# Kernel tuning notes

Measured on AMD Instinct MI355X. Metric: run time of the kernel, lower is better.

## Reference

```python
import jax, jax.numpy as jnp
import numpy as np
import math

D_MODEL = 1024
N_HEAD = 16
FFN_HIDDEN = 4096
EPS = 1e-12


def _layernorm(x, gamma, beta):
    # faithful to repo: unbiased std (ddof=1), divide by (std + eps)
    mean = jnp.mean(x, axis=-1, keepdims=True)
    std = jnp.std(x, axis=-1, keepdims=True, ddof=1)
    return gamma * ((x - mean) / (std + EPS)) + beta


def setup_inputs() -> dict:
    key = jax.random.key(0)
    ks = jax.random.split(key, 12)
    B, L, D, H = 2, 2048, D_MODEL, FFN_HIDDEN
    s = 0.02
    inp = {
        "x": jax.random.normal(ks[0], (B, L, D), dtype=jnp.float32),
        "src_mask": jnp.ones((B, 1, 1, L), dtype=jnp.int32),
        "wq_w": jax.random.normal(ks[1], (D, D), jnp.float32) * s,
        "wq_b": jnp.zeros((D,), jnp.float32),
        "wk_w": jax.random.normal(ks[2], (D, D), jnp.float32) * s,
        "wk_b": jnp.zeros((D,), jnp.float32),
        "wv_w": jax.random.normal(ks[3], (D, D), jnp.float32) * s,
        "wv_b": jnp.zeros((D,), jnp.float32),
        "wo_w": jax.random.normal(ks[4], (D, D), jnp.float32) * s,
        "wo_b": jnp.zeros((D,), jnp.float32),
        "gamma1": jnp.ones((D,), jnp.float32),
        "beta1": jnp.zeros((D,), jnp.float32),
        "ff1_w": jax.random.normal(ks[5], (D, H), jnp.float32) * s,
        "ff1_b": jnp.zeros((H,), jnp.float32),
        "ff2_w": jax.random.normal(ks[6], (H, D), jnp.float32) * s,
        "ff2_b": jnp.zeros((D,), jnp.float32),
        "gamma2": jnp.ones((D,), jnp.float32),
        "beta2": jnp.zeros((D,), jnp.float32),
    }
    return inp


def _encoder_layer(x, src_mask, wq_w, wq_b, wk_w, wk_b, wv_w, wv_b, wo_w, wo_b,
                   gamma1, beta1, ff1_w, ff1_b, ff2_w, ff2_b, gamma2, beta2):
    B, L, D = x.shape
    H = N_HEAD
    d_t = D // H
    # projections
    q = x @ wq_w + wq_b
    k = x @ wk_w + wk_b
    v = x @ wv_w + wv_b
    # faithful .view() split: reshape [B,L,D] -> [B,H,L,d_t] (no transpose)
    q = q.reshape(B, H, L, d_t)
    k = k.reshape(B, H, L, d_t)
    v = v.reshape(B, H, L, d_t)
    score = jnp.einsum("bhqd,bhkd->bhqk", q, k) / math.sqrt(d_t)
    score = jnp.where(src_mask == 0, jnp.float32(-1e-12), score)
    score = jax.nn.softmax(score, axis=-1)
    out = jnp.einsum("bhqk,bhkd->bhqd", score, v)
    out = out.reshape(B, L, D)  # faithful .view() concat
    attn = out @ wo_w + wo_b
    # residual + LN1 (dropout p=0)
    x1 = _layernorm(attn + x, gamma1, beta1)
    # FFN
    ff = jax.nn.relu(x1 @ ff1_w + ff1_b) @ ff2_w + ff2_b
    return _layernorm(ff + x1, gamma2, beta2)


def reference(x, src_mask, wq_w, wq_b, wk_w, wk_b, wv_w, wv_b, wo_w, wo_b,
              gamma1, beta1, ff1_w, ff1_b, ff2_w, ff2_b, gamma2, beta2):
    return _encoder_layer(x, src_mask, wq_w, wq_b, wk_w, wk_b, wv_w, wv_b,
                          wo_w, wo_b, gamma1, beta1, ff1_w, ff1_b, ff2_w,
                          ff2_b, gamma2, beta2)
```

## Files before the change

### kernel.cpp

```cpp
#include <hip/hip_runtime.h>
#include <hip/hip_bf16.h>
#include <cstdint>
#include <cstddef>

using bf16 = __hip_bfloat16;
typedef __attribute__((ext_vector_type(8))) short short8v;
typedef __attribute__((ext_vector_type(4))) short short4v;
typedef __attribute__((ext_vector_type(4))) float float4v;

__device__ inline float b2f(short s) {
  union { float f; uint32_t u; } z; z.u = ((uint32_t)(uint16_t)s) << 16; return z.f;
}
__device__ inline short f2b(float f) {
  bf16 h = __float2bfloat16(f);
  return *reinterpret_cast<short*>(&h);
}

typedef const __attribute__((address_space(1))) uint32_t* gas1p;
typedef __attribute__((address_space(3))) uint32_t* las3p;
__device__ inline void gload_lds16(const void* g, void* l) {
  __builtin_amdgcn_global_load_lds((gas1p)g, (las3p)l, 16, 0, 0);
}

__global__ __launch_bounds__(256) void gemm_bt(
    const bf16* __restrict__ A, const bf16* __restrict__ Bt,
    const float* __restrict__ bias, void* __restrict__ C,
    int M, int N, int K, int ldc, int relu_mode, int out_f32) {
  __shared__ __align__(16) bf16 As[128 * 32];
  __shared__ __align__(16) bf16 Bs[128 * 32];
  const int tid = threadIdx.x;
  const int w = tid >> 6, lane = tid & 63;
  const int quad = lane >> 4, l16 = lane & 15;
  const int wrow = (w >> 1) * 64, wcol = (w & 1) * 64;
  const int mbase = blockIdx.y * 128, nbase = blockIdx.x * 128;
  const int c = w * 128 + lane;
  const int row0 = c >> 2, p0 = c & 3;
  const int row1 = (c + 64) >> 2, p1 = (c + 64) & 3;

  float4v acc[4][4];
  for (int i = 0; i < 4; i++)
    for (int j = 0; j < 4; j++) acc[i][j] = (float4v){0.f, 0.f, 0.f, 0.f};

  for (int k0 = 0; k0 < K; k0 += 32) {
    __syncthreads();
    gload_lds16(A + (size_t)(mbase + row0) * K + k0 + p0 * 8, (char*)As + w * 2048);
    gload_lds16(A + (size_t)(mbase + row1) * K + k0 + p1 * 8, (char*)As + w * 2048 + 1024);
    gload_lds16(Bt + (size_t)(nbase + row0) * K + k0 + p0 * 8, (char*)Bs + w * 2048);
    gload_lds16(Bt + (size_t)(nbase + row1) * K + k0 + p1 * 8, (char*)Bs + w * 2048 + 1024);
    __syncthreads();

    short8v a[4], b[4];
    for (int mt = 0; mt < 4; mt++)
      a[mt] = *reinterpret_cast<const short8v*>(As + (wrow + mt * 16 + l16) * 32 + quad * 8);
    for (int nt = 0; nt < 4; nt++)
      b[nt] = *reinterpret_cast<const short8v*>(Bs + (wcol + nt * 16 + l16) * 32 + quad * 8);
    for (int mt = 0; mt < 4; mt++)
      for (int nt = 0; nt < 4; nt++)
        acc[mt][nt] = __builtin_amdgcn_mfma_f32_16x16x32_bf16(a[mt], b[nt], acc[mt][nt], 0, 0, 0);
  }

  for (int nt = 0; nt < 4; nt++) {
    int col = nbase + wcol + nt * 16 + l16;
    float bv = bias[col];
    for (int mt = 0; mt < 4; mt++) {
      int row = mbase + wrow + mt * 16 + quad * 4;
      for (int r = 0; r < 4; r++) {
        float v = acc[mt][nt][r] + bv;
        if (relu_mode) v = fmaxf(v, 0.f);
        size_t idx = (size_t)(row + r) * ldc + col;
        if (out_f32) ((float*)C)[idx] = v;
        else         ((short*)C)[idx] = f2b(v);
      }
    }
  }
}

__global__ __launch_bounds__(256) void attn_kernel(
    const bf16* __restrict__ qkv, const int* __restrict__ mask,
    bf16* __restrict__ ao) {
  __shared__ __align__(16) short Vt[2][64 * 40];
  __shared__ __align__(16) short Pbuf[4][32 * 40];

  const int tid = threadIdx.x;
  const int w = tid >> 6, lane = tid & 63;
  const int quad = lane >> 4, l16 = lane & 15;
  const int bh = blockIdx.y, b = bh >> 4;
  const int row0 = bh * 128;
  const int qbase = blockIdx.x * 128 + w * 32;
  const int vr = tid & 31, vdb = (tid >> 5) * 8;

  short8v aq[2][2];
  for (int h = 0; h < 2; h++)
    for (int dh = 0; dh < 2; dh++) {
      int local = (qbase + h * 16 + l16) * 64 + dh * 32 + quad * 8;
      aq[h][dh] = *reinterpret_cast<const short8v*>(
          qkv + (size_t)(row0 + (local >> 10)) * 3072 + (local & 1023));
    }

  const bf16* pk[2][2];
  for (int s = 0; s < 2; s++)
    for (int dh = 0; dh < 2; dh++) {
      int local = (s * 16 + l16) * 64 + dh * 32 + quad * 8;
      pk[s][dh] = qkv + (size_t)(row0 + (local >> 10)) * 3072 + (local & 1023) + 1024;
    }
  const bf16* pv;
  {
    int local = vr * 64 + vdb;
    pv = qkv + (size_t)(row0 + (local >> 10)) * 3072 + (local & 1023) + 2048;
  }
  const int* pm = mask + b * 2048 + quad * 4;

  float4v o[2][4];
  for (int h = 0; h < 2; h++)
    for (int nt = 0; nt < 4; nt++) o[h][nt] = (float4v){0.f, 0.f, 0.f, 0.f};
  float lsum[2] = {0.f, 0.f};

  short8v kcur[2][2], vcur;
  vcur = *reinterpret_cast<const short8v*>(pv);
  for (int s = 0; s < 2; s++)
    for (int dh = 0; dh < 2; dh++)
      kcur[s][dh] = *reinterpret_cast<const short8v*>(pk[s][dh]);
  int4 mc0 = *reinterpret_cast<const int4*>(pm);
  int4 mc1 = *reinterpret_cast<const int4*>(pm + 16);
  pv += 6144; pm += 32;
  for (int s = 0; s < 2; s++)
    for (int dh = 0; dh < 2; dh++) pk[s][dh] += 6144;
  {
    short* vt = &Vt[0][0];
    for (int j = 0; j < 8; j++) vt[(vdb + j) * 40 + vr] = vcur[j];
  }
  __syncthreads();

  for (int it = 0; it < 64; it++) {
    const int pb = it & 1;
    short8v knext[2][2], vnext;
    int4 mn0, mn1;
    if (it < 63) {
      vnext = *reinterpret_cast<const short8v*>(pv);
      for (int s = 0; s < 2; s++)
        for (int dh = 0; dh < 2; dh++)
          knext[s][dh] = *reinterpret_cast<const short8v*>(pk[s][dh]);
      mn0 = *reinterpret_cast<const int4*>(pm);
      mn1 = *reinterpret_cast<const int4*>(pm + 16);
      pv += 6144; pm += 32;
      for (int s = 0; s < 2; s++)
        for (int dh = 0; dh < 2; dh++) pk[s][dh] += 6144;
    }

    float4v st[2][2];
    for (int s = 0; s < 2; s++)
      for (int h = 0; h < 2; h++) {
        float4v t = (float4v){0.f, 0.f, 0.f, 0.f};
        t = __builtin_amdgcn_mfma_f32_16x16x32_bf16(kcur[s][0], aq[h][0], t, 0, 0, 0);
        t = __builtin_amdgcn_mfma_f32_16x16x32_bf16(kcur[s][1], aq[h][1], t, 0, 0, 0);
        st[s][h] = t;
      }

    for (int h = 0; h < 2; h++)
      for (int s = 0; s < 2; s++) {
        int4 mv = s ? mc1 : mc0;
        int mm[4] = {mv.x, mv.y, mv.z, mv.w};
        short4v pkv;
        for (int r = 0; r < 4; r++) {
          float y = st[s][h][r] * 0.180336880f;
          y = fminf(fmaxf(y, -43.3f), 43.3f);
          y = (mm[r] == 0) ? -1.4427e-12f : y;
          float e = __builtin_amdgcn_exp2f(y);
          lsum[h] += e;
          pkv[r] = f2b(e);
        }
        *reinterpret_cast<short4v*>(&Pbuf[w][(h * 16 + l16) * 40 + s * 16 + quad * 4]) = pkv;
      }
    short8v pf[2];
    for (int h = 0; h < 2; h++)
      pf[h] = *reinterpret_cast<const short8v*>(&Pbuf[w][(h * 16 + l16) * 40 + quad * 8]);
    for (int nt = 0; nt < 4; nt++) {
      short8v bv = *reinterpret_cast<const short8v*>(&Vt[pb][(nt * 16 + l16) * 40 + quad * 8]);
      for (int h = 0; h < 2; h++)
        o[h][nt] = __builtin_amdgcn_mfma_f32_16x16x32_bf16(pf[h], bv, o[h][nt], 0, 0, 0);
    }

    if (it < 63) {
      short* vt = &Vt[1 - pb][0];
      for (int j = 0; j < 8; j++) vt[(vdb + j) * 40 + vr] = vnext[j];
      for (int s = 0; s < 2; s++)
        for (int dh = 0; dh < 2; dh++) kcur[s][dh] = knext[s][dh];
      mc0 = mn0; mc1 = mn1;
    }
    __syncthreads();
  }

  for (int h = 0; h < 2; h++) {
    lsum[h] += __shfl_xor(lsum[h], 16);
    lsum[h] += __shfl_xor(lsum[h], 32);
  }
  for (int h = 0; h < 2; h++)
    for (int r = 0; r < 4; r++) {
      float linv = 1.0f / __shfl(lsum[h], quad * 4 + r);
      int qg = qbase + h * 16 + quad * 4 + r;
      for (int nt = 0; nt < 4; nt++) {
        int d = nt * 16 + l16;
        ao[(size_t)bh * 131072 + (size_t)qg * 64 + d] = __float2bfloat16(o[h][nt][r] * linv);
      }
    }
}

__global__ __launch_bounds__(256) void ln_resid(
    const void* __restrict__ a, const void* __restrict__ xres,
    const float* __restrict__ gamma, const float* __restrict__ beta,
    void* __restrict__ out, int a_f32, int x_f32, int out_f32) {
  __shared__ float red[8];
  const int row = blockIdx.x, tid = threadIdx.x;
  const int w = tid >> 6, lane = tid & 63;
  const size_t base = (size_t)row * 1024;
  float v[4]; float sum = 0.f, ss = 0.f;
  for (int i = 0; i < 4; i++) {
    int c = tid + i * 256;
    float av = a_f32 ? ((const float*)a)[base + c] : b2f(((const short*)a)[base + c]);
    float xv = x_f32 ? ((const float*)xres)[base + c] : b2f(((const short*)xres)[base + c]);
    v[i] = av + xv;
    sum += v[i]; ss += v[i] * v[i];
  }
  for (int off = 1; off < 64; off <<= 1) {
    sum += __shfl_xor(sum, off);
    ss  += __shfl_xor(ss, off);
  }
  if (lane == 0) { red[w * 2] = sum; red[w * 2 + 1] = ss; }
  __syncthreads();
  sum = red[0] + red[2] + red[4] + red[6];
  ss  = red[1] + red[3] + red[5] + red[7];
  float mean = sum * (1.0f / 1024.0f);
  float var = (ss - 1024.0f * mean * mean) * (1.0f / 1023.0f);
  var = fmaxf(var, 0.f);
  float rden = 1.0f / (sqrtf(var) + 1e-12f);
  for (int i = 0; i < 4; i++) {
    int c = tid + i * 256;
    float y = gamma[c] * ((v[i] - mean) * rden) + beta[c];
    if (out_f32) ((float*)out)[base + c] = y;
    else         ((short*)out)[base + c] = f2b(y);
  }
}

__global__ __launch_bounds__(256) void transpose_k(
    const float* __restrict__ in, bf16* __restrict__ out, int R, int C) {
  __shared__ short t[32][33];
  const int tx = threadIdx.x, ty = threadIdx.y;
  const int cb = blockIdx.x * 32, rb = blockIdx.y * 32;
  for (int j = 0; j < 4; j++)
    t[ty + j * 8][tx] = f2b(in[(size_t)(rb + ty + j * 8) * C + cb + tx]);
  __syncthreads();
  for (int j = 0; j < 4; j++)
    ((short*)out)[(size_t)(cb + ty + j * 8) * R + rb + tx] = t[tx][ty + j * 8];
}

__global__ __launch_bounds__(256) void concat3(
    const float* __restrict__ a, const float* __restrict__ b,
    const float* __restrict__ c, float* __restrict__ out) {
  int i = blockIdx.x * 256 + threadIdx.x;
  float v;
  if (i < 1024)       v = a[i];
  else if (i < 2048)  v = b[i - 1024];
  else                v = c[i - 2048];
  out[i] = v;
}

__global__ __launch_bounds__(256) void cast_f32_bf16(
    const float* __restrict__ in, bf16* __restrict__ out) {
  int i0 = (blockIdx.x * 256 + threadIdx.x) * 4;
  float4 f = *reinterpret_cast<const float4*>(in + i0);
  short* o = (short*)out + i0;
  o[0] = f2b(f.x); o[1] = f2b(f.y); o[2] = f2b(f.z); o[3] = f2b(f.w);
}

extern "C" void kernel_launch(void* const* d_in, const int* in_sizes, int n_in,
                              void* d_out, int out_size, void* d_ws, size_t ws_size,
                              hipStream_t stream) {
  (void)in_sizes; (void)n_in; (void)out_size; (void)ws_size;
  const float* x    = (const float*)d_in[0];
  const int*   mask = (const int*)d_in[1];
  const float* wq_w = (const float*)d_in[2];
  const float* wq_b = (const float*)d_in[3];
  const float* wk_w = (const float*)d_in[4];
  const float* wk_b = (const float*)d_in[5];
  const float* wv_w = (const float*)d_in[6];
  const float* wv_b = (const float*)d_in[7];
  const float* wo_w = (const float*)d_in[8];
  const float* wo_b = (const float*)d_in[9];
  const float* g1   = (const float*)d_in[10];
  const float* be1  = (const float*)d_in[11];
  const float* f1w  = (const float*)d_in[12];
  const float* f1b  = (const float*)d_in[13];
  const float* f2w  = (const float*)d_in[14];
  const float* f2b_ = (const float*)d_in[15];
  const float* g2   = (const float*)d_in[16];
  const float* be2  = (const float*)d_in[17];
  float* out = (float*)d_out;
  char* ws = (char*)d_ws;

  bf16*  QKV  = (bf16*)(ws + 0);
  bf16*  Xbf  = (bf16*)(ws + 25165824);
  bf16*  AO   = (bf16*)(ws + 25165824);
  bf16*  PROJ = (bf16*)(ws + 0);
  bf16*  H    = (bf16*)(ws + 0);
  bf16*  X1   = (bf16*)(ws + 33554432);
  bf16*  WT   = (bf16*)(ws + 41943040);
  float* BQKV = (float*)(ws + 48234496);

  dim3 tb(32, 8);
  cast_f32_bf16<<<dim3(4096), dim3(256), 0, stream>>>(x, Xbf);
  transpose_k<<<dim3(32, 32), tb, 0, stream>>>(wq_w, WT, 1024, 1024);
  transpose_k<<<dim3(32, 32), tb, 0, stream>>>(wk_w, WT + 1024 * 1024, 1024, 1024);
  transpose_k<<<dim3(32, 32), tb, 0, stream>>>(wv_w, WT + 2 * 1024 * 1024, 1024, 1024);
  concat3<<<dim3(12), dim3(256), 0, stream>>>(wq_b, wk_b, wv_b, BQKV);
  gemm_bt<<<dim3(24, 32), dim3(256), 0, stream>>>(Xbf, WT, BQKV, QKV, 4096, 3072, 1024, 3072, 0, 0);
  attn_kernel<<<dim3(16, 32), dim3(256), 0, stream>>>(QKV, mask, AO);
  transpose_k<<<dim3(32, 32), tb, 0, stream>>>(wo_w, WT, 1024, 1024);
  gemm_bt<<<dim3(8, 32), dim3(256), 0, stream>>>(AO, WT, wo_b, PROJ, 4096, 1024, 1024, 1024, 0, 0);
  ln_resid<<<dim3(4096), dim3(256), 0, stream>>>(PROJ, x, g1, be1, X1, 0, 1, 0);
  transpose_k<<<dim3(128, 32), tb, 0, stream>>>(f1w, WT, 1024, 4096);
  gemm_bt<<<dim3(32, 32), dim3(256), 0, stream>>>(X1, WT, f1b, H, 4096, 4096, 1024, 4096, 1, 0);
  transpose_k<<<dim3(32, 128), tb, 0, stream>>>(f2w, WT, 4096, 1024);
  gemm_bt<<<dim3(8, 32), dim3(256), 0, stream>>>(H, WT, f2b_, out, 4096, 1024, 4096, 1024, 0, 1);
  ln_resid<<<dim3(4096), dim3(256), 0, stream>>>(out, X1, g2, be2, out, 1, 0, 1);
}
```

Measured before the change: 474.1 us.

## Split-K the output and FFN2 GEMMs with atomic accumulation into f32

Adds a double-buffered register-prefetch GEMM kernel that splits the K dimension across two z-blocks and accumulates partial tiles with float atomicAdd into an f32 buffer pre-filled with bias. It is used for the attention output projection and the second FFN GEMM, whose 8x32 grids give only 256 blocks. The intent is to double the block count on these narrow-N GEMMs and overlap global loads with MFMA work. The cost is extra bias-init launches, atomic traffic, f32 intermediates instead of bf16 for the projection, and non-deterministic summation order.

```diff
diff --git a/kernel.cpp b/kernel.cpp
--- a/kernel.cpp
+++ b/kernel.cpp
@@ -73,6 +73,86 @@
       }
     }
   }
+}
+
+__global__ __launch_bounds__(256) void gemm_pipe(
+    const bf16* __restrict__ A, const bf16* __restrict__ Bt,
+    float* __restrict__ C, int K, int ldc, int k_len) {
+  __shared__ __align__(16) bf16 As[2][128 * 32];
+  __shared__ __align__(16) bf16 Bs[2][128 * 32];
+  const int tid = threadIdx.x;
+  const int w = tid >> 6, lane = tid & 63;
+  const int quad = lane >> 4, l16 = lane & 15;
+  const int wrow = (w >> 1) * 64, wcol = (w & 1) * 64;
+  const int mbase = blockIdx.y * 128, nbase = blockIdx.x * 128;
+  const int srow = tid >> 1, scol = (tid & 1) * 16;
+
+  const bf16* ag = A + (size_t)(mbase + srow) * K + blockIdx.z * k_len + scol;
+  const bf16* bg = Bt + (size_t)(nbase + srow) * K + blockIdx.z * k_len + scol;
+
+  float4v acc[4][4];
+  for (int i = 0; i < 4; i++)
+    for (int j = 0; j < 4; j++) acc[i][j] = (float4v){0.f, 0.f, 0.f, 0.f};
+
+  {
+    short8v a0 = *reinterpret_cast<const short8v*>(ag);
+    short8v a1 = *reinterpret_cast<const short8v*>(ag + 8);
+    short8v b0 = *reinterpret_cast<const short8v*>(bg);
+    short8v b1 = *reinterpret_cast<const short8v*>(bg + 8);
+    *reinterpret_cast<short8v*>(&As[0][srow * 32 + scol])     = a0;
+    *reinterpret_cast<short8v*>(&As[0][srow * 32 + scol + 8]) = a1;
+    *reinterpret_cast<short8v*>(&Bs[0][srow * 32 + scol])     = b0;
+    *reinterpret_cast<short8v*>(&Bs[0][srow * 32 + scol + 8]) = b1;
+  }
+  __syncthreads();
+
+  const int KT = k_len >> 5;
+  for (int kt = 0; kt < KT; kt++) {
+    const int pb = kt & 1;
+    short8v na0, na1, nb0, nb1;
+    const bool more = (kt + 1 < KT);
+    if (more) {
+      const bf16* ap = ag + (kt + 1) * 32;
+      const bf16* bp = bg + (kt + 1) * 32;
+      na0 = *reinterpret_cast<const short8v*>(ap);
+      na1 = *reinterpret_cast<const short8v*>(ap + 8);
+      nb0 = *reinterpret_cast<const short8v*>(bp);
+      nb1 = *reinterpret_cast<const short8v*>(bp + 8);
+    }
+
+    short8v a[4], b[4];
+    for (int mt = 0; mt < 4; mt++)
+      a[mt] = *reinterpret_cast<const short8v*>(&As[pb][(wrow + mt * 16 + l16) * 32 + quad * 8]);
+    for (int nt = 0; nt < 4; nt++)
+      b[nt] = *reinterpret_cast<const short8v*>(&Bs[pb][(wcol + nt * 16 + l16) * 32 + quad * 8]);
+    for (int mt = 0; mt < 4; mt++)
+      for (int nt = 0; nt < 4; nt++)
+        acc[mt][nt] = __builtin_amdgcn_mfma_f32_16x16x32_bf16(a[mt], b[nt], acc[mt][nt], 0, 0, 0);
+
+    if (more) {
+      *reinterpret_cast<short8v*>(&As[1 - pb][srow * 32 + scol])     = na0;
+      *reinterpret_cast<short8v*>(&As[1 - pb][srow * 32 + scol + 8]) = na1;
+      *reinterpret_cast<short8v*>(&Bs[1 - pb][srow * 32 + scol])     = nb0;
+      *reinterpret_cast<short8v*>(&Bs[1 - pb][srow * 32 + scol + 8]) = nb1;
+    }
+    __syncthreads();
+  }
+
+  for (int nt = 0; nt < 4; nt++) {
+    int col = nbase + wcol + nt * 16 + l16;
+    for (int mt = 0; mt < 4; mt++) {
+      int row = mbase + wrow + mt * 16 + quad * 4;
+      for (int r = 0; r < 4; r++)
+        atomicAdd(&C[(size_t)(row + r) * ldc + col], acc[mt][nt][r]);
+    }
+  }
+}
+
+__global__ __launch_bounds__(256) void bias_init(
+    const float* __restrict__ bias, float* __restrict__ C) {
+  int c = threadIdx.x * 4;
+  float4 bv = *reinterpret_cast<const float4*>(bias + c);
+  *reinterpret_cast<float4*>(C + (size_t)blockIdx.x * 1024 + c) = bv;
 }
 
 __global__ __launch_bounds__(256) void attn_kernel(
@@ -300,7 +380,7 @@
   bf16*  QKV  = (bf16*)(ws + 0);
   bf16*  Xbf  = (bf16*)(ws + 25165824);
   bf16*  AO   = (bf16*)(ws + 25165824);
-  bf16*  PROJ = (bf16*)(ws + 0);
+  float* PROJ = (float*)(ws + 0);
   bf16*  H    = (bf16*)(ws + 0);
   bf16*  X1   = (bf16*)(ws + 33554432);
   bf16*  WT   = (bf16*)(ws + 41943040);
@@ -315,11 +395,13 @@
   gemm_bt<<<dim3(24, 32), dim3(256), 0, stream>>>(Xbf, WT, BQKV, QKV, 4096, 3072, 1024, 3072, 0, 0);
   attn_kernel<<<dim3(16, 32), dim3(256), 0, stream>>>(QKV, mask, AO);
   transpose_k<<<dim3(32, 32), tb, 0, stream>>>(wo_w, WT, 1024, 1024);
-  gemm_bt<<<dim3(8, 32), dim3(256), 0, stream>>>(AO, WT, wo_b, PROJ, 4096, 1024, 1024, 1024, 0, 0);
-  ln_resid<<<dim3(4096), dim3(256), 0, stream>>>(PROJ, x, g1, be1, X1, 0, 1, 0);
+  bias_init<<<dim3(4096), dim3(256), 0, stream>>>(wo_b, PROJ);
+  gemm_pipe<<<dim3(8, 32, 2), dim3(256), 0, stream>>>(AO, WT, PROJ, 1024, 1024, 512);
+  ln_resid<<<dim3(4096), dim3(256), 0, stream>>>(PROJ, x, g1, be1, X1, 1, 1, 0);
   transpose_k<<<dim3(128, 32), tb, 0, stream>>>(f1w, WT, 1024, 4096);
   gemm_bt<<<dim3(32, 32), dim3(256), 0, stream>>>(X1, WT, f1b, H, 4096, 4096, 1024, 4096, 1, 0);
   transpose_k<<<dim3(32, 128), tb, 0, stream>>>(f2w, WT, 4096, 1024);
-  gemm_bt<<<dim3(8, 32), dim3(256), 0, stream>>>(H, WT, f2b_, out, 4096, 1024, 4096, 1024, 0, 1);
+  bias_init<<<dim3(4096), dim3(256), 0, stream>>>(f2b_, out);
+  gemm_pipe<<<dim3(8, 32, 2), dim3(256), 0, stream>>>(H, WT, out, 4096, 1024, 2048);
   ln_resid<<<dim3(4096), dim3(256), 0, stream>>>(out, X1, g2, be2, out, 1, 0, 1);
 }
```

Result: no change. 473.6 us (-0.1%).
